# Performance work log

Measured on AMD Instinct MI355X. Metric: run time of the kernel, lower is better.

## Reference

```python
import jax, jax.numpy as jnp
import numpy as np

B, CIN, COUT, H, W, K = 4, 64, 64, 128, 128, 3
KK = K * K


def setup_inputs() -> dict:
    key = jax.random.key(0)
    k1, k2, k3, k4 = jax.random.split(key, 4)
    x = jax.random.normal(k1, (B, CIN, H, W), dtype=jnp.float32)
    offset = jax.random.normal(k2, (B, 2 * KK, H, W), dtype=jnp.float32)
    mask = jax.random.uniform(k3, (B, KK, H, W), dtype=jnp.float32)
    n = CIN * KK
    stdv = 1.0 / np.sqrt(n)
    weight = jax.random.uniform(k4, (COUT, CIN, K, K), dtype=jnp.float32,
                                minval=-stdv, maxval=stdv)
    bias = jnp.zeros((COUT,), dtype=jnp.float32)
    return {"x": x, "offset": offset, "mask": mask, "weight": weight, "bias": bias}


def _sample(x, ci, cj):
    # x: (b,c,h,w); ci,cj: (b,h,w,kk) int32 -> (b,c,h,w,kk), zero outside bounds
    b, c, h, w = x.shape
    valid = (ci >= 0) & (ci < h) & (cj >= 0) & (cj < w)  # (b,h,w,kk)
    idx = jnp.clip(ci, 0, h - 1) * w + jnp.clip(cj, 0, w - 1)
    flat = x.reshape(b, c, h * w)
    g = jnp.take_along_axis(flat, idx.reshape(b, 1, -1), axis=2)
    g = g.reshape(b, c, h, w, -1)
    return jnp.where(valid[:, None], g, jnp.zeros((), x.dtype))


def reference(x, offset, mask, weight, bias):
    b, c, h, w = x.shape
    # offset: (b, kk*2, h, w) -> (b, h, w, kk, 2)
    off = offset.reshape(b, KK, 2, h, w).transpose(0, 3, 4, 1, 2)
    # base sampling grid: coord[i,j,ki,kj] = (i-1+ki, j-1+kj), flattened over kk
    di, dj = jnp.meshgrid(jnp.arange(-(K // 2), K // 2 + 1),
                          jnp.arange(-(K // 2), K // 2 + 1), indexing='ij')
    base_i = jnp.arange(h, dtype=jnp.float32)[:, None, None] + di.reshape(1, 1, KK)
    base_j = jnp.arange(w, dtype=jnp.float32)[None, :, None] + dj.reshape(1, 1, KK)
    coord_i = off[..., 0] + base_i  # (b,h,w,kk)
    coord_j = off[..., 1] + base_j

    lt_i = jnp.floor(coord_i)
    lt_j = jnp.floor(coord_j)
    rb_i = jnp.ceil(coord_i)
    rb_j = jnp.ceil(coord_j)
    li, lj = lt_i.astype(jnp.int32), lt_j.astype(jnp.int32)
    ri, rj = rb_i.astype(jnp.int32), rb_j.astype(jnp.int32)

    v_lt = _sample(x, li, lj)
    v_rb = _sample(x, ri, rj)
    v_rt = _sample(x, li, rj)
    v_lb = _sample(x, ri, lj)

    # bilinear fractions, broadcast over channel dim
    fi = (coord_i - lt_i)[:, None]  # (b,1,h,w,kk)
    fj = (coord_j - lt_j)[:, None]
    v_t = v_lt + fj * (v_rt - v_lt)
    v_b = v_lb + fj * (v_rb - v_lb)
    v = v_t + fi * (v_b - v_t)  # (b,c,h,w,kk)

    # modulation mask: (b,kk,h,w) -> (b,1,h,w,kk)
    v = v * mask.transpose(0, 2, 3, 1)[:, None]

    w_flat = weight.reshape(weight.shape[0], c, KK)
    out = jnp.einsum('oik,bihwk->bohw', w_flat, v)
    return out + bias[None, :, None, None]
```

## Files before the change

kernel.cpp:

```cpp
#include <hip/hip_runtime.h>

#define B_   4
#define CIN  64
#define COUT 64
#define H_   128
#define W_   128
#define HW   (H_*W_)
#define KK   9
#define ROWS_R 16
#define COLS_R 24
#define OFFB  (ROWS_R * COLS_R * 128)
#define SMEMB (OFFB + 27 * 128 * 4)
#define NBLK 512

typedef short bf16x8 __attribute__((ext_vector_type(8)));
typedef float f32x4  __attribute__((ext_vector_type(4)));
typedef float f32x2  __attribute__((ext_vector_type(2)));
typedef unsigned int u32;
typedef unsigned int u32x4 __attribute__((ext_vector_type(4)));

__device__ __forceinline__ unsigned short f2bf(float f) {
    unsigned int u = __float_as_uint(f);
    u = (u + 0x7FFFu + ((u >> 16) & 1u)) >> 16;
    return (unsigned short)u;
}

__global__ __launch_bounds__(256) void k_transpose(const float* __restrict__ x,
                                                   unsigned short* __restrict__ xt) {
    __shared__ float lds[64 * 129];
    int bi = blockIdx.x;
    int b = bi >> 7, i = bi & 127;
    int tid = threadIdx.x;
#pragma unroll
    for (int cc = 0; cc < 32; ++cc) {
        int c = cc * 2 + (tid >> 7);
        int w = tid & 127;
        lds[c * 129 + w] = x[((b * CIN + c) * H_ + i) * W_ + w];
    }
    __syncthreads();
#pragma unroll
    for (int q = 0; q < 32; ++q) {
        int c = tid & 63;
        int w = q * 4 + (tid >> 6);
        xt[((b * H_ + i) * W_ + w) * CIN + c] = f2bf(lds[c * 129 + w]);
    }
}

__global__ __launch_bounds__(256) void k_weight(const float* __restrict__ w,
                                                unsigned short* __restrict__ wtf) {
    int t = blockIdx.x * 256 + threadIdx.x;
    if (t >= 18 * 4 * 64 * 8) return;
    int j    = t & 7;
    int lane = (t >> 3) & 63;
    int nt   = (t >> 9) & 3;
    int s    = t >> 11;
    int kg   = s * 32 + ((lane >> 4) << 3) + j;
    int n    = nt * 16 + (lane & 15);
    int kpos = kg >> 6, c = kg & 63;
    wtf[t] = f2bf(w[(n * CIN + c) * 9 + kpos]);
}

__global__ __launch_bounds__(512, 4) void k_main(
    const unsigned short* __restrict__ xt,
    const float* __restrict__ offset,
    const float* __restrict__ mask,
    const unsigned short* __restrict__ wtf,
    const float* __restrict__ bias,
    float* __restrict__ out) {
    __shared__ __align__(16) unsigned char smem[SMEMB];

    const int tid  = threadIdx.x;
    const int lane = tid & 63;
    const int wv   = tid >> 6;
    const int T  = ((blockIdx.x & 7) << 6) + (blockIdx.x >> 3);
    const int b  = T >> 7;
    const int i0 = ((T >> 3) & 15) * 8;
    const int j0 = (T & 7) * 16;
    const char* xb = (const char*)xt + (size_t)b * HW * 128;

    {
        const int iA = i0 - 4, jA = j0 - 4;
#pragma unroll
        for (int k = 0; k < 6; ++k) {
            int idx = k * 512 + tid;
            int rec = idx >> 3, c = idx & 7;
            int rr = rec / COLS_R, cc = rec - rr * COLS_R;
            int gr = min(max(iA + rr, 0), H_ - 1);
            int gc = min(max(jA + cc, 0), W_ - 1);
            u32x4 v = *(const u32x4*)(xb + (((gr << 7) + gc) << 7) + (c << 4));
            *(u32x4*)(smem + (rec << 7) + (((c + rec) & 7) << 4)) = v;
        }
    }
    {
        const float* op = offset + (size_t)b * 18 * HW;
        const float* mp = mask   + (size_t)b * 9  * HW;
#pragma unroll
        for (int k = 0; k < 2; ++k) {
            int idx = k * 512 + tid;
            if (idx < 864) {
                int q = idx >> 5, rem = idx & 31;
                int row = rem >> 2, c4 = (rem & 3) << 2;
                const float* src = (q < 18 ? op + q * HW : mp + (q - 18) * HW)
                                   + (i0 + row) * W_ + j0 + c4;
                *(f32x4*)(smem + OFFB + idx * 16) = *(const f32x4*)src;
            }
        }
    }
    __syncthreads();

    const int p  = lane & 15;
    const int g  = lane >> 4;
    const int ir = i0 + wv;
    const int jc = j0 + p;
    const float* offl = (const float*)(smem + OFFB);
    float offv[18], mskv[9];
#pragma unroll
    for (int q = 0; q < 18; ++q) offv[q] = offl[q * 128 + wv * 16 + p];
#pragma unroll
    for (int q = 0; q < 9; ++q)  mskv[q] = offl[(18 + q) * 128 + wv * 16 + p];

    const bf16x8* wp = (const bf16x8*)wtf;
    f32x4 acc0 = {0,0,0,0}, acc1 = {0,0,0,0}, acc2 = {0,0,0,0}, acc3 = {0,0,0,0};

#pragma unroll
    for (int kp = 0; kp < 9; ++kp) {
        float oi  = offv[2 * kp];
        float oj  = offv[2 * kp + 1];
        float msk = mskv[kp];
        float ci = oi + (float)(ir + kp / 3 - 1);
        float cj = oj + (float)(jc + kp % 3 - 1);
        float fli = floorf(ci), flj = floorf(cj);
        float fi = ci - fli, fj = cj - flj;
        int li = (int)fli, lj = (int)flj;
        int li1 = li + 1, lj1 = lj + 1;
        float vy0 = (li  >= 0 && li  < H_) ? 1.f : 0.f;
        float vy1 = (li1 >= 0 && li1 < H_) ? 1.f : 0.f;
        float vx0 = (lj  >= 0 && lj  < W_) ? 1.f : 0.f;
        float vx1 = (lj1 >= 0 && lj1 < W_) ? 1.f : 0.f;
        float gi = fi * msk, gj = fj * msk;
        float w11 = gi * fj;
        f32x4 w4;
        w4.x = (msk - gi - gj + w11) * vy0 * vx0;
        w4.y = (gj - w11) * vy0 * vx1;
        w4.z = (gi - w11) * vy1 * vx0;
        w4.w = w11 * vy1 * vx1;
        int y0 = min(max(li,  0), H_ - 1), y1 = min(max(li1, 0), H_ - 1);
        int x0 = min(max(lj,  0), W_ - 1), x1 = min(max(lj1, 0), W_ - 1);
        int a00 = ((y0 << 7) + x0) << 7, a01 = ((y0 << 7) + x1) << 7;
        int a10 = ((y1 << 7) + x0) << 7, a11 = ((y1 << 7) + x1) << 7;
        int rli = li - (i0 - 4), rlj = lj - (j0 - 4);
        bool inr = ((unsigned)rli <= (unsigned)(ROWS_R - 2)) &&
                   ((unsigned)rlj <= (unsigned)(COLS_R - 2));
        int rli_c = min(max(rli, 0), ROWS_R - 2), rlj_c = min(max(rlj, 0), COLS_R - 2);
        int r00 = rli_c * COLS_R + rlj_c;
        int r01 = r00 + 1, r10 = r00 + COLS_R, r11 = r00 + COLS_R + 1;

#pragma unroll
        for (int h = 0; h < 2; ++h) {
            int ch = h * 4 + g;
            u32x4 q00 = *(const u32x4*)(smem + (r00 << 7) + (((ch + r00) & 7) << 4));
            u32x4 q01 = *(const u32x4*)(smem + (r01 << 7) + (((ch + r01) & 7) << 4));
            u32x4 q10 = *(const u32x4*)(smem + (r10 << 7) + (((ch + r10) & 7) << 4));
            u32x4 q11 = *(const u32x4*)(smem + (r11 << 7) + (((ch + r11) & 7) << 4));
            if (!inr) {
                int c = (g << 4) + (h << 6);
                q00 = *(const u32x4*)(xb + a00 + c);
                q01 = *(const u32x4*)(xb + a01 + c);
                q10 = *(const u32x4*)(xb + a10 + c);
                q11 = *(const u32x4*)(xb + a11 + c);
            }
            f32x2 wx = {w4.x, w4.x}, wy = {w4.y, w4.y};
            f32x2 wz = {w4.z, w4.z}, ww = {w4.w, w4.w};
            u32x4 po;
#pragma unroll
            for (int q = 0; q < 4; ++q) {
                f32x2 c00 = {__uint_as_float(q00[q] << 16), __uint_as_float(q00[q] & 0xFFFF0000u)};
                f32x2 c01 = {__uint_as_float(q01[q] << 16), __uint_as_float(q01[q] & 0xFFFF0000u)};
                f32x2 c10 = {__uint_as_float(q10[q] << 16), __uint_as_float(q10[q] & 0xFFFF0000u)};
                f32x2 c11 = {__uint_as_float(q11[q] << 16), __uint_as_float(q11[q] & 0xFFFF0000u)};
                f32x2 r = wx * c00 + wy * c01 + wz * c10 + ww * c11;
                po[q] = __builtin_amdgcn_perm(__float_as_uint(r.y) + 0x8000u,
                                              __float_as_uint(r.x) + 0x8000u, 0x07060302u);
            }
            bf16x8 af; *(u32x4*)&af = po;
            int s = kp * 2 + h;
            acc0 = __builtin_amdgcn_mfma_f32_16x16x32_bf16(af, wp[(s*4+0)*64 + lane], acc0, 0, 0, 0);
            acc1 = __builtin_amdgcn_mfma_f32_16x16x32_bf16(af, wp[(s*4+1)*64 + lane], acc1, 0, 0, 0);
            acc2 = __builtin_amdgcn_mfma_f32_16x16x32_bf16(af, wp[(s*4+2)*64 + lane], acc2, 0, 0, 0);
            acc3 = __builtin_amdgcn_mfma_f32_16x16x32_bf16(af, wp[(s*4+3)*64 + lane], acc3, 0, 0, 0);
        }
    }

    __syncthreads();
    float* cst = (float*)smem;
    {
        f32x4 v0 = acc0, v1 = acc1, v2 = acc2, v3 = acc3;
        float bs0 = bias[p], bs1 = bias[16 + p], bs2 = bias[32 + p], bs3 = bias[48 + p];
#pragma unroll
        for (int r = 0; r < 4; ++r) { v0[r] += bs0; v1[r] += bs1; v2[r] += bs2; v3[r] += bs3; }
        const int pm = wv * 16 + (g << 2);
        *(f32x4*)&cst[(p)      * 132 + pm] = v0;
        *(f32x4*)&cst[(16 + p) * 132 + pm] = v1;
        *(f32x4*)&cst[(32 + p) * 132 + pm] = v2;
        *(f32x4*)&cst[(48 + p) * 132 + pm] = v3;
    }
    __syncthreads();
    const size_t obase = (size_t)b * (COUT * HW) + i0 * W_ + j0;
#pragma unroll
    for (int k = 0; k < 4; ++k) {
        int idx = k * 512 + tid;
        int cout = idx >> 5, chunk = idx & 31;
        int row = chunk >> 2, col = (chunk & 3) << 2;
        f32x4 vv = *(const f32x4*)&cst[cout * 132 + chunk * 4];
        __builtin_nontemporal_store(vv,
            (f32x4*)&out[obase + (size_t)cout * HW + row * W_ + col]);
    }
}

extern "C" void kernel_launch(void* const* d_in, const int* in_sizes, int n_in,
                              void* d_out, int out_size, void* d_ws, size_t ws_size,
                              hipStream_t stream) {
    const float* x      = (const float*)d_in[0];
    const float* offset = (const float*)d_in[1];
    const float* mask   = (const float*)d_in[2];
    const float* weight = (const float*)d_in[3];
    const float* bias   = (const float*)d_in[4];
    float* out = (float*)d_out;
    unsigned short* xt  = (unsigned short*)d_ws;
    unsigned short* wtf = xt + (size_t)B_ * H_ * W_ * CIN;

    k_transpose<<<B_ * H_, 256, 0, stream>>>(x, xt);
    k_weight<<<144, 256, 0, stream>>>(weight, wtf);
    k_main<<<NBLK, 512, 0, stream>>>(xt, offset, mask, wtf, bias, out);
}
```

Baseline: 37.98 us.

## Shrink LDS halo and raise occupancy by loading offsets on demand

Reduces the staged input halo from 4 to 3 pixels, which shrinks the LDS tile and the number of cooperative load iterations. Offsets and mask are read from LDS inside the tap loop instead of being preloaded into 27 registers, and the launch bound rises to 6 blocks per CU to increase occupancy. The gather loads for both channel halves are issued together before the conversion, with the global fallback also batched. The smaller halo sends more samples with large offsets down the slow global-memory path, and the extra LDS reads and register pressure may offset the occupancy gain.

```diff
diff --git a/kernel.cpp b/kernel.cpp
--- a/kernel.cpp
+++ b/kernel.cpp
@@ -7,10 +7,12 @@
 #define W_   128
 #define HW   (H_*W_)
 #define KK   9
-#define ROWS_R 16
-#define COLS_R 24
-#define OFFB  (ROWS_R * COLS_R * 128)
-#define SMEMB (OFFB + 27 * 128 * 4)
+#define HALO 3
+#define ROWS_R (8 + 2*HALO)
+#define COLS_R (16 + 2*HALO)
+#define RECS   (ROWS_R * COLS_R)
+#define OFFB   (RECS * 128)
+#define SMEMB  (OFFB + 27 * 128 * 4)
 #define NBLK 512
 
 typedef short bf16x8 __attribute__((ext_vector_type(8)));
@@ -60,7 +62,7 @@
     wtf[t] = f2bf(w[(n * CIN + c) * 9 + kpos]);
 }
 
-__global__ __launch_bounds__(512, 4) void k_main(
+__global__ __launch_bounds__(512, 6) void k_main(
     const unsigned short* __restrict__ xt,
     const float* __restrict__ offset,
     const float* __restrict__ mask,
@@ -79,16 +81,18 @@
     const char* xb = (const char*)xt + (size_t)b * HW * 128;
 
     {
-        const int iA = i0 - 4, jA = j0 - 4;
-#pragma unroll
-        for (int k = 0; k < 6; ++k) {
+        const int iA = i0 - HALO, jA = j0 - HALO;
+#pragma unroll
+        for (int k = 0; k < 5; ++k) {
             int idx = k * 512 + tid;
-            int rec = idx >> 3, c = idx & 7;
-            int rr = rec / COLS_R, cc = rec - rr * COLS_R;
-            int gr = min(max(iA + rr, 0), H_ - 1);
-            int gc = min(max(jA + cc, 0), W_ - 1);
-            u32x4 v = *(const u32x4*)(xb + (((gr << 7) + gc) << 7) + (c << 4));
-            *(u32x4*)(smem + (rec << 7) + (((c + rec) & 7) << 4)) = v;
+            if (idx < RECS * 8) {
+                int rec = idx >> 3, c = idx & 7;
+                int rr = rec / COLS_R, cc = rec - rr * COLS_R;
+                int gr = min(max(iA + rr, 0), H_ - 1);
+                int gc = min(max(jA + cc, 0), W_ - 1);
+                u32x4 v = *(const u32x4*)(xb + (((gr << 7) + gc) << 7) + (c << 4));
+                *(u32x4*)(smem + (rec << 7) + (((c + rec) & 7) << 4)) = v;
+            }
         }
     }
     {
@@ -112,21 +116,15 @@
     const int g  = lane >> 4;
     const int ir = i0 + wv;
     const int jc = j0 + p;
-    const float* offl = (const float*)(smem + OFFB);
-    float offv[18], mskv[9];
-#pragma unroll
-    for (int q = 0; q < 18; ++q) offv[q] = offl[q * 128 + wv * 16 + p];
-#pragma unroll
-    for (int q = 0; q < 9; ++q)  mskv[q] = offl[(18 + q) * 128 + wv * 16 + p];
-
+    const float* offl = (const float*)(smem + OFFB) + wv * 16 + p;
     const bf16x8* wp = (const bf16x8*)wtf;
     f32x4 acc0 = {0,0,0,0}, acc1 = {0,0,0,0}, acc2 = {0,0,0,0}, acc3 = {0,0,0,0};
 
 #pragma unroll
     for (int kp = 0; kp < 9; ++kp) {
-        float oi  = offv[2 * kp];
-        float oj  = offv[2 * kp + 1];
-        float msk = mskv[kp];
+        float oi  = offl[(2 * kp) * 128];
+        float oj  = offl[(2 * kp + 1) * 128];
+        float msk = offl[(18 + kp) * 128];
         float ci = oi + (float)(ir + kp / 3 - 1);
         float cj = oj + (float)(jc + kp % 3 - 1);
         float fli = floorf(ci), flj = floorf(cj);
@@ -148,36 +146,43 @@
         int x0 = min(max(lj,  0), W_ - 1), x1 = min(max(lj1, 0), W_ - 1);
         int a00 = ((y0 << 7) + x0) << 7, a01 = ((y0 << 7) + x1) << 7;
         int a10 = ((y1 << 7) + x0) << 7, a11 = ((y1 << 7) + x1) << 7;
-        int rli = li - (i0 - 4), rlj = lj - (j0 - 4);
+        int rli = li - (i0 - HALO), rlj = lj - (j0 - HALO);
         bool inr = ((unsigned)rli <= (unsigned)(ROWS_R - 2)) &&
                    ((unsigned)rlj <= (unsigned)(COLS_R - 2));
         int rli_c = min(max(rli, 0), ROWS_R - 2), rlj_c = min(max(rlj, 0), COLS_R - 2);
         int r00 = rli_c * COLS_R + rlj_c;
         int r01 = r00 + 1, r10 = r00 + COLS_R, r11 = r00 + COLS_R + 1;
 
+        u32x4 q00[2], q01[2], q10[2], q11[2];
 #pragma unroll
         for (int h = 0; h < 2; ++h) {
             int ch = h * 4 + g;
-            u32x4 q00 = *(const u32x4*)(smem + (r00 << 7) + (((ch + r00) & 7) << 4));
-            u32x4 q01 = *(const u32x4*)(smem + (r01 << 7) + (((ch + r01) & 7) << 4));
-            u32x4 q10 = *(const u32x4*)(smem + (r10 << 7) + (((ch + r10) & 7) << 4));
-            u32x4 q11 = *(const u32x4*)(smem + (r11 << 7) + (((ch + r11) & 7) << 4));
-            if (!inr) {
+            q00[h] = *(const u32x4*)(smem + (r00 << 7) + (((ch + r00) & 7) << 4));
+            q01[h] = *(const u32x4*)(smem + (r01 << 7) + (((ch + r01) & 7) << 4));
+            q10[h] = *(const u32x4*)(smem + (r10 << 7) + (((ch + r10) & 7) << 4));
+            q11[h] = *(const u32x4*)(smem + (r11 << 7) + (((ch + r11) & 7) << 4));
+        }
+        if (!inr) {
+#pragma unroll
+            for (int h = 0; h < 2; ++h) {
                 int c = (g << 4) + (h << 6);
-                q00 = *(const u32x4*)(xb + a00 + c);
-                q01 = *(const u32x4*)(xb + a01 + c);
-                q10 = *(const u32x4*)(xb + a10 + c);
-                q11 = *(const u32x4*)(xb + a11 + c);
-            }
-            f32x2 wx = {w4.x, w4.x}, wy = {w4.y, w4.y};
-            f32x2 wz = {w4.z, w4.z}, ww = {w4.w, w4.w};
+                q00[h] = *(const u32x4*)(xb + a00 + c);
+                q01[h] = *(const u32x4*)(xb + a01 + c);
+                q10[h] = *(const u32x4*)(xb + a10 + c);
+                q11[h] = *(const u32x4*)(xb + a11 + c);
+            }
+        }
+        f32x2 wx = {w4.x, w4.x}, wy = {w4.y, w4.y};
+        f32x2 wz = {w4.z, w4.z}, ww = {w4.w, w4.w};
+#pragma unroll
+        for (int h = 0; h < 2; ++h) {
             u32x4 po;
 #pragma unroll
             for (int q = 0; q < 4; ++q) {
-                f32x2 c00 = {__uint_as_float(q00[q] << 16), __uint_as_float(q00[q] & 0xFFFF0000u)};
-                f32x2 c01 = {__uint_as_float(q01[q] << 16), __uint_as_float(q01[q] & 0xFFFF0000u)};
-                f32x2 c10 = {__uint_as_float(q10[q] << 16), __uint_as_float(q10[q] & 0xFFFF0000u)};
-                f32x2 c11 = {__uint_as_float(q11[q] << 16), __uint_as_float(q11[q] & 0xFFFF0000u)};
+                f32x2 c00 = {__uint_as_float(q00[h][q] << 16), __uint_as_float(q00[h][q] & 0xFFFF0000u)};
+                f32x2 c01 = {__uint_as_float(q01[h][q] << 16), __uint_as_float(q01[h][q] & 0xFFFF0000u)};
+                f32x2 c10 = {__uint_as_float(q10[h][q] << 16), __uint_as_float(q10[h][q] & 0xFFFF0000u)};
+                f32x2 c11 = {__uint_as_float(q11[h][q] << 16), __uint_as_float(q11[h][q] & 0xFFFF0000u)};
                 f32x2 r = wx * c00 + wy * c01 + wz * c10 + ww * c11;
                 po[q] = __builtin_amdgcn_perm(__float_as_uint(r.y) + 0x8000u,
                                               __float_as_uint(r.x) + 0x8000u, 0x07060302u);
```

Measured after the change: 35.57 us. -6.3%, faster.
